# Kernel optimization log

Measured on AMD Instinct MI355X. Metric: run time of the kernel, lower is better.

The kernel has to match this reference:

```python
import jax, jax.numpy as jnp
import numpy as np


def _to_complex(x):
    # trailing axis holds (real, imag)
    return x[..., 0] + 1j * x[..., 1]


def _nufft2c(img, omega, csm):
    """Exact type-2 non-uniform DFT with coil sensitivities (reference for nufft2c_torch).

    img:   (H, W) real or complex image
    omega: (2, M) k-space coords in cycles/pixel, in [-0.5, 0.5]
    csm:   (C, H, W) complex coil sensitivity maps
    returns (C, M) complex k-space, centered & orthonormal-style 1/sqrt(HW) scaling.
    """
    H, W = img.shape
    y = jnp.arange(H, dtype=jnp.float32) - H / 2.0  # centered pixel coords
    z = jnp.arange(W, dtype=jnp.float32) - W / 2.0
    ey = jnp.exp(-2j * jnp.pi * omega[0][:, None] * y[None, :])  # (M, H)
    ez = jnp.exp(-2j * jnp.pi * omega[1][:, None] * z[None, :])  # (M, W)
    sim = csm * img[None, :, :].astype(csm.dtype)                # (C, H, W)
    tmp = jnp.einsum('chw,mw->cmh', sim, ez)                     # (C, M, H)
    k = jnp.einsum('cmh,mh->cm', tmp, ey) / np.float32(np.sqrt(H * W))
    return k


def setup_inputs() -> dict:
    key = jax.random.key(0)
    k0, k1, k2, k3, k4 = jax.random.split(key, 5)
    H = W = 300
    C = 4       # coils
    M = 4096    # non-Cartesian k-space samples
    img_pred = jax.random.normal(k0, (H, W, 1), jnp.float32)
    kdata = jax.random.normal(k1, (1, C, M, 2), jnp.float32)
    all_omega = jax.random.uniform(k2, (1, 2, M), jnp.float32) - 0.5  # cycles/pixel
    all_dcomp = jax.random.uniform(k3, (1, M), jnp.float32)
    all_csm = jax.random.normal(k4, (C, H, W, 2), jnp.float32)
    return {
        'img_pred': img_pred,
        'kdata': kdata,
        'all_omega': all_omega,
        'all_dcomp': all_dcomp,
        'all_csm': all_csm,
    }


def reference(img_pred, kdata, all_omega, all_dcomp, all_csm):
    Ncontrast = 1
    csm = _to_complex(all_csm)   # (C, H, W)
    kd = _to_complex(kdata)      # (Ncontrast, C, M)
    two_pi = jnp.float32(2.0 * np.pi)
    # radial k-space weighting, (Ncontrast, M)
    weight = jnp.sqrt((all_omega[:, 0, :] * two_pi) ** 2 +
                      (all_omega[:, 1, :] * two_pi) ** 2) + 1.0
    loss = jnp.float32(0.0)
    for ii in range(Ncontrast):
        img = img_pred[:, :, ii]                       # (H, W)
        ksp = _nufft2c(img, all_omega[ii], csm)        # (C, M)
        d = weight[ii][None, :] * (ksp - kd[ii])       # weighted complex residual
        # MSELoss over view_as_real == mean over all real & imag components
        loss = loss + jnp.mean(jnp.stack([d.real, d.imag]) ** 2)
    return loss
```

## Files before the change

kernel.cpp:

```cpp
#include <hip/hip_runtime.h>
#include <math.h>

#define HH 300
#define WW 300
#define CC 4
#define MM 4096
#define KP 640
#define NKC (KP/32)
#define CSTRIDE 384
#define MP (CC*CSTRIDE)
#define NP 8192
#define NRB (MP/128)

typedef __attribute__((ext_vector_type(4))) float f32x4;
typedef __attribute__((ext_vector_type(4))) int int4v;
typedef __attribute__((ext_vector_type(8))) int int8v;

#define TWO_PI 6.283185307179586f


__global__ __launch_bounds__(256) void prep_kernel(
    const float* __restrict__ img, const float* __restrict__ csm,
    const float* __restrict__ omega, unsigned char* __restrict__ A,
    unsigned char* __restrict__ B, float* __restrict__ out)
{
    const int bid = blockIdx.x;
    const int t   = threadIdx.x;
    if (bid == 0 && t == 0) out[0] = 0.0f;
    const int lane = t & 63;
    const int jj   = lane & 7;
    const int rl   = lane >> 3;

    if (bid < 960) {
        int gw = (bid * 256 + t) >> 6;
        int kc = gw / 192;
        int row = (gw - kc * 192) * 8 + rl;
        int k0 = kc * 32 + jj * 4;
        unsigned int word = 0;
        int c = row / CSTRIDE;
        int h = row - c * CSTRIDE;
        if (h < HH) {
            float v[4];
            #pragma unroll
            for (int q = 0; q < 4; ++q) {
                int k = k0 + q;
                float vv = 0.0f;
                if (k < 2 * WW) {
                    int w = (k < WW) ? k : k - WW;
                    float im = img[h * WW + w];
                    const float* cs = csm + (((size_t)c * HH + h) * WW + w) * 2;
                    vv = ((k < WW) ? cs[0] : cs[1]) * im;
                }
                v[q] = vv;
            }
            unsigned int lo = (unsigned int)(ushort)__builtin_amdgcn_cvt_pk_fp8_f32(v[0], v[1], 0, false);
            unsigned int hi = (unsigned int)(ushort)__builtin_amdgcn_cvt_pk_fp8_f32(v[2], v[3], 0, false);
            word = lo | (hi << 16);
        }
        *(unsigned int*)(A + ((size_t)kc * MP + row) * 32 + jj * 4) = word;
    } else {
        int gw = ((bid - 960) * 256 + t) >> 6;
        int kc = gw / 512;
        int m  = (gw - kc * 512) * 8 + rl;
        int k0 = kc * 32 + jj * 4;
        float om1 = omega[MM + m];
        float p0[4], p1[4];
        #pragma unroll
        for (int q = 0; q < 4; ++q) {
            int k = k0 + q;
            float a0 = 0.0f, a1 = 0.0f;
            if (k < 2 * WW) {
                int w = (k < WW) ? k : k - WW;
                float s, c;
                __sincosf(TWO_PI * om1 * (float)(w - 150), &s, &c);
                a0 = (k < WW) ? c : s;
                a1 = (k < WW) ? -s : c;
            }
            p0[q] = a0; p1[q] = a1;
        }
        unsigned int lo0 = (unsigned int)(ushort)__builtin_amdgcn_cvt_pk_fp8_f32(p0[0], p0[1], 0, false);
        unsigned int hi0 = (unsigned int)(ushort)__builtin_amdgcn_cvt_pk_fp8_f32(p0[2], p0[3], 0, false);
        unsigned int lo1 = (unsigned int)(ushort)__builtin_amdgcn_cvt_pk_fp8_f32(p1[0], p1[1], 0, false);
        unsigned int hi1 = (unsigned int)(ushort)__builtin_amdgcn_cvt_pk_fp8_f32(p1[2], p1[3], 0, false);
        *(unsigned int*)(B + ((size_t)kc * NP + m) * 32 + jj * 4)      = lo0 | (hi0 << 16);
        *(unsigned int*)(B + ((size_t)kc * NP + m + MM) * 32 + jj * 4) = lo1 | (hi1 << 16);
    }
}

__global__ __launch_bounds__(256, 3) void gemm_kernel(
    const unsigned char* __restrict__ A, const unsigned char* __restrict__ B,
    const float* __restrict__ omega, float2* __restrict__ P)
{
    __shared__ float2 red[128];

    const int t    = threadIdx.x;
    const int wave = t >> 6;
    const int ln   = t & 63;
    const int row0 = blockIdx.y * 128;
    const int col0 = blockIdx.x * 128;
    const int wr = wave >> 1, wc = wave & 1;
    const int lr = ln & 15;
    const int lq = ln >> 4;

    if (t < 128) red[t] = make_float2(0.0f, 0.0f);

    const int arow = row0 + wr * 64 + lr;
    const int bcol = col0 + wc * 64 + lr;

    f32x4 acc[4][4] = {};

    #pragma unroll
    for (int kc = 0; kc < NKC; kc += 4) {
        int8v a[4], b[4];
        #pragma unroll
        for (int i = 0; i < 4; ++i) {
            const unsigned char* pA = A + ((size_t)(kc + lq) * MP + arow + i * 16) * 32;
            int4v lo = *(const int4v*)pA;
            int4v hi = *(const int4v*)(pA + 16);
            a[i] = __builtin_shufflevector(lo, hi, 0, 1, 2, 3, 4, 5, 6, 7);
        }
        #pragma unroll
        for (int j = 0; j < 4; ++j) {
            const unsigned char* pB = B + ((size_t)(kc + lq) * NP + bcol + j * 16) * 32;
            int4v lo = *(const int4v*)pB;
            int4v hi = *(const int4v*)(pB + 16);
            b[j] = __builtin_shufflevector(lo, hi, 0, 1, 2, 3, 4, 5, 6, 7);
        }
        #pragma unroll
        for (int i = 0; i < 4; ++i)
            #pragma unroll
            for (int j = 0; j < 4; ++j)
                acc[i][j] = __builtin_amdgcn_mfma_scale_f32_16x16x128_f8f6f4(
                    a[i], b[j], acc[i][j], 0, 0,
                    0, 0x7f7f7f7f, 0, 0x7f7f7f7f);
    }

    __syncthreads();

    const int c  = row0 / CSTRIDE;
    const int h0 = row0 - c * CSTRIDE;

    #pragma unroll
    for (int j = 0; j < 4; ++j) {
        const int jcol = wc * 64 + j * 16 + lr;
        const int m = (col0 + jcol) & (MM - 1);
        const float om0 = omega[m];
        float ss, sc;
        __sincosf(TWO_PI * om0, &ss, &sc);
        const float str = sc, sti = -ss;
        float s2r = str * str - sti * sti, s2i = 2.0f * str * sti;
        float s4r = s2r * s2r - s2i * s2i, s4i = 2.0f * s2r * s2i;
        float s8r = s4r * s4r - s4i * s4i, s8i = 2.0f * s4r * s4i;
        float s16r = s8r * s8r - s8i * s8i, s16i = 2.0f * s8r * s8i;

        const int hb0 = h0 + wr * 64 + lq * 4;
        float sn, cs;
        __sincosf(TWO_PI * om0 * (float)(hb0 - 150), &sn, &cs);
        float byr = cs, byi = -sn;

        float pr = 0.0f, pi = 0.0f;
        #pragma unroll
        for (int i = 0; i < 4; ++i) {
            float er = byr, ei = byi;
            #pragma unroll
            for (int r = 0; r < 4; ++r) {
                const float v = acc[i][j][r];
                pr = fmaf(v, er, pr);
                pi = fmaf(v, ei, pi);
                float nr = er * str - ei * sti;
                ei = er * sti + ei * str;
                er = nr;
            }
            float nbr = byr * s16r - byi * s16i;
            byi = byr * s16i + byi * s16r;
            byr = nbr;
        }
        pr += __shfl_down(pr, 32); pi += __shfl_down(pi, 32);
        pr += __shfl_down(pr, 16); pi += __shfl_down(pi, 16);
        if (lq == 0) {
            atomicAdd(&red[jcol].x, pr);
            atomicAdd(&red[jcol].y, pi);
        }
    }
    __syncthreads();

    if (t < 128) {
        const int rb = row0 >> 7;
        P[(size_t)rb * NP + col0 + t] = red[t];
    }
}

__global__ __launch_bounds__(64) void loss_kernel(
    const float2* __restrict__ P, const float* __restrict__ kdata,
    const float* __restrict__ omega, float* __restrict__ out)
{
    const int t = blockIdx.x * 64 + threadIdx.x;
    const int c = t >> 12;
    const int m = t & (MM - 1);

    float kr = 0.0f, ki = 0.0f;
    #pragma unroll
    for (int q = 0; q < 3; ++q) {
        const int rb = 3 * c + q;
        float2 p0 = P[(size_t)rb * NP + m];
        float2 p1 = P[(size_t)rb * NP + m + MM];
        kr += p0.x - p1.y;
        ki += p0.y + p1.x;
    }
    kr *= (1.0f / 300.0f);
    ki *= (1.0f / 300.0f);

    const float om0 = omega[m];
    const float om1 = omega[MM + m];
    const size_t kidx = ((size_t)c * MM + m) * 2;
    const float kdr = kdata[kidx];
    const float kdi = kdata[kidx + 1];
    const float w0 = om0 * TWO_PI, w1 = om1 * TWO_PI;
    const float wg = sqrtf(w0 * w0 + w1 * w1) + 1.0f;
    const float dr = wg * (kr - kdr);
    const float di = wg * (ki - kdi);
    float val = (dr * dr + di * di) * (1.0f / (2.0f * CC * MM));

    #pragma unroll
    for (int off = 32; off > 0; off >>= 1) val += __shfl_down(val, off);
    if (threadIdx.x == 0) atomicAdd(out, val);
}

extern "C" void kernel_launch(void* const* d_in, const int* in_sizes, int n_in,
                              void* d_out, int out_size, void* d_ws, size_t ws_size,
                              hipStream_t stream) {
    const float* img   = (const float*)d_in[0];
    const float* kdata = (const float*)d_in[1];
    const float* omega = (const float*)d_in[2];
    const float* csm   = (const float*)d_in[4];
    float* out = (float*)d_out;

    unsigned char* Aws = (unsigned char*)d_ws;
    unsigned char* Bws = (unsigned char*)d_ws + (1u << 20);
    float2*        Pws = (float2*)((char*)d_ws + (8u << 20));

    prep_kernel<<<960 + 2560, 256, 0, stream>>>(img, csm, omega, Aws, Bws, out);
    gemm_kernel<<<dim3(NP / 128, MP / 128), 256, 0, stream>>>(Aws, Bws, omega, Pws);
    loss_kernel<<<CC * MM / 64, 64, 0, stream>>>(Pws, kdata, omega, out);
}
```

Before: 86.30 us.

## Use single-wave 64x64 GEMM blocks and skip padded row blocks

The GEMM now runs one wave per block on 64x64 tiles. It iterates over only 20 of the 24 row blocks, skipping the all-zero padding block (rows 320-383) of each coil. Each wave writes its partial sums directly to P, which removes the shared-memory atomics and both block barriers. The loss kernel now sums 5 partial blocks per coil instead of 3. The cost is less data reuse per block (A and B tiles are fetched by more blocks) in exchange for less padded work and more, smaller blocks.

```diff
diff --git a/kernel.cpp b/kernel.cpp
--- a/kernel.cpp
+++ b/kernel.cpp
@@ -10,7 +10,6 @@
 #define CSTRIDE 384
 #define MP (CC*CSTRIDE)
 #define NP 8192
-#define NRB (MP/128)
 
 typedef __attribute__((ext_vector_type(4))) float f32x4;
 typedef __attribute__((ext_vector_type(4))) int int4v;
@@ -87,25 +86,17 @@
     }
 }
 
-__global__ __launch_bounds__(256, 3) void gemm_kernel(
+__global__ __launch_bounds__(64, 4) void gemm_kernel(
     const unsigned char* __restrict__ A, const unsigned char* __restrict__ B,
     const float* __restrict__ omega, float2* __restrict__ P)
 {
-    __shared__ float2 red[128];
-
-    const int t    = threadIdx.x;
-    const int wave = t >> 6;
-    const int ln   = t & 63;
-    const int row0 = blockIdx.y * 128;
-    const int col0 = blockIdx.x * 128;
-    const int wr = wave >> 1, wc = wave & 1;
-    const int lr = ln & 15;
-    const int lq = ln >> 4;
-
-    if (t < 128) red[t] = make_float2(0.0f, 0.0f);
-
-    const int arow = row0 + wr * 64 + lr;
-    const int bcol = col0 + wc * 64 + lr;
+    const int ln   = threadIdx.x;
+    const int lr   = ln & 15;
+    const int lq   = ln >> 4;
+    const int y    = blockIdx.y;
+    const int rbp  = y + y / 5;
+    const int row0 = rbp * 64;
+    const int col0 = blockIdx.x * 64;
 
     f32x4 acc[4][4] = {};
 
@@ -114,14 +105,14 @@
         int8v a[4], b[4];
         #pragma unroll
         for (int i = 0; i < 4; ++i) {
-            const unsigned char* pA = A + ((size_t)(kc + lq) * MP + arow + i * 16) * 32;
+            const unsigned char* pA = A + ((size_t)(kc + lq) * MP + row0 + i * 16 + lr) * 32;
             int4v lo = *(const int4v*)pA;
             int4v hi = *(const int4v*)(pA + 16);
             a[i] = __builtin_shufflevector(lo, hi, 0, 1, 2, 3, 4, 5, 6, 7);
         }
         #pragma unroll
         for (int j = 0; j < 4; ++j) {
-            const unsigned char* pB = B + ((size_t)(kc + lq) * NP + bcol + j * 16) * 32;
+            const unsigned char* pB = B + ((size_t)(kc + lq) * NP + col0 + j * 16 + lr) * 32;
             int4v lo = *(const int4v*)pB;
             int4v hi = *(const int4v*)(pB + 16);
             b[j] = __builtin_shufflevector(lo, hi, 0, 1, 2, 3, 4, 5, 6, 7);
@@ -135,15 +126,12 @@
                     0, 0x7f7f7f7f, 0, 0x7f7f7f7f);
     }
 
-    __syncthreads();
-
-    const int c  = row0 / CSTRIDE;
-    const int h0 = row0 - c * CSTRIDE;
+    const int h0 = (rbp % 6) * 64;
 
     #pragma unroll
     for (int j = 0; j < 4; ++j) {
-        const int jcol = wc * 64 + j * 16 + lr;
-        const int m = (col0 + jcol) & (MM - 1);
+        const int col = col0 + j * 16 + lr;
+        const int m = col & (MM - 1);
         const float om0 = omega[m];
         float ss, sc;
         __sincosf(TWO_PI * om0, &ss, &sc);
@@ -153,7 +141,7 @@
         float s8r = s4r * s4r - s4i * s4i, s8i = 2.0f * s4r * s4i;
         float s16r = s8r * s8r - s8i * s8i, s16i = 2.0f * s8r * s8i;
 
-        const int hb0 = h0 + wr * 64 + lq * 4;
+        const int hb0 = h0 + lq * 4;
         float sn, cs;
         __sincosf(TWO_PI * om0 * (float)(hb0 - 150), &sn, &cs);
         float byr = cs, byi = -sn;
@@ -177,16 +165,8 @@
         }
         pr += __shfl_down(pr, 32); pi += __shfl_down(pi, 32);
         pr += __shfl_down(pr, 16); pi += __shfl_down(pi, 16);
-        if (lq == 0) {
-            atomicAdd(&red[jcol].x, pr);
-            atomicAdd(&red[jcol].y, pi);
-        }
-    }
-    __syncthreads();
-
-    if (t < 128) {
-        const int rb = row0 >> 7;
-        P[(size_t)rb * NP + col0 + t] = red[t];
+        if (lq == 0)
+            P[(size_t)y * NP + col] = make_float2(pr, pi);
     }
 }
 
@@ -200,10 +180,10 @@
 
     float kr = 0.0f, ki = 0.0f;
     #pragma unroll
-    for (int q = 0; q < 3; ++q) {
-        const int rb = 3 * c + q;
-        float2 p0 = P[(size_t)rb * NP + m];
-        float2 p1 = P[(size_t)rb * NP + m + MM];
+    for (int q = 0; q < 5; ++q) {
+        const int y = 5 * c + q;
+        float2 p0 = P[(size_t)y * NP + m];
+        float2 p1 = P[(size_t)y * NP + m + MM];
         kr += p0.x - p1.y;
         ki += p0.y + p1.x;
     }
@@ -240,6 +220,6 @@
     float2*        Pws = (float2*)((char*)d_ws + (8u << 20));
 
     prep_kernel<<<960 + 2560, 256, 0, stream>>>(img, csm, omega, Aws, Bws, out);
-    gemm_kernel<<<dim3(NP / 128, MP / 128), 256, 0, stream>>>(Aws, Bws, omega, Pws);
+    gemm_kernel<<<dim3(NP / 64, 20), 64, 0, stream>>>(Aws, Bws, omega, Pws);
     loss_kernel<<<CC * MM / 64, 64, 0, stream>>>(Pws, kdata, omega, out);
 }
```

New measurement: 97.76 us. +13.3%, slower.

## Store FP8 operands in MFMA fragment order for coalesced 16-byte loads

Applied to the files above, without the earlier changes.

The prep kernel now writes A and B in a per-fragment layout: each 16-row by 128-k block occupies 2048 contiguous bytes arranged so each lane's two 16-byte halves sit at ln*16 and ln*16+1024. The GEMM loads each operand fragment as two fully contiguous wave-wide 1KB reads instead of strided 32-byte rows per k-chunk, which is meant to improve global/L2 access efficiency. The GEMM launch bound also drops the min-3-blocks occupancy hint, giving the compiler more register freedom at the risk of lower occupancy.

```diff
diff --git a/kernel.cpp b/kernel.cpp
--- a/kernel.cpp
+++ b/kernel.cpp
@@ -6,11 +6,12 @@
 #define CC 4
 #define MM 4096
 #define KP 640
-#define NKC (KP/32)
+#define NKG (KP/128)
 #define CSTRIDE 384
 #define MP (CC*CSTRIDE)
 #define NP 8192
 #define NRB (MP/128)
+#define BHALF (2621440)
 
 typedef __attribute__((ext_vector_type(4))) float f32x4;
 typedef __attribute__((ext_vector_type(4))) int int4v;
@@ -27,18 +28,23 @@
     const int bid = blockIdx.x;
     const int t   = threadIdx.x;
     if (bid == 0 && t == 0) out[0] = 0.0f;
-    const int lane = t & 63;
-    const int jj   = lane & 7;
-    const int rl   = lane >> 3;
 
     if (bid < 960) {
-        int gw = (bid * 256 + t) >> 6;
-        int kc = gw / 192;
-        int row = (gw - kc * 192) * 8 + rl;
-        int k0 = kc * 32 + jj * 4;
+        const int gid = bid * 256 + t;
+        const int L   = gid * 4;
+        const int fragidx = L >> 11;
+        const int o  = L & 2047;
+        const int hf = (o >> 10) & 1;
+        const int ch = (o >> 8) & 3;
+        const int lr = (o >> 4) & 15;
+        const int b0 = o & 15;
+        const int row16 = fragidx / NKG;
+        const int g     = fragidx - row16 * NKG;
+        const int row = row16 * 16 + lr;
+        const int k0  = g * 128 + ch * 32 + hf * 16 + b0;
+        const int c = row / CSTRIDE;
+        const int h = row - c * CSTRIDE;
         unsigned int word = 0;
-        int c = row / CSTRIDE;
-        int h = row - c * CSTRIDE;
         if (h < HH) {
             float v[4];
             #pragma unroll
@@ -57,13 +63,21 @@
             unsigned int hi = (unsigned int)(ushort)__builtin_amdgcn_cvt_pk_fp8_f32(v[2], v[3], 0, false);
             word = lo | (hi << 16);
         }
-        *(unsigned int*)(A + ((size_t)kc * MP + row) * 32 + jj * 4) = word;
+        *(unsigned int*)(A + L) = word;
     } else {
-        int gw = ((bid - 960) * 256 + t) >> 6;
-        int kc = gw / 512;
-        int m  = (gw - kc * 512) * 8 + rl;
-        int k0 = kc * 32 + jj * 4;
-        float om1 = omega[MM + m];
+        const int gid = (bid - 960) * 256 + t;
+        const int L   = gid * 4;
+        const int fragidx = L >> 11;
+        const int o  = L & 2047;
+        const int hf = (o >> 10) & 1;
+        const int ch = (o >> 8) & 3;
+        const int lr = (o >> 4) & 15;
+        const int b0 = o & 15;
+        const int m16 = fragidx / NKG;
+        const int g   = fragidx - m16 * NKG;
+        const int m  = m16 * 16 + lr;
+        const int k0 = g * 128 + ch * 32 + hf * 16 + b0;
+        const float om1 = omega[MM + m];
         float p0[4], p1[4];
         #pragma unroll
         for (int q = 0; q < 4; ++q) {
@@ -82,12 +96,12 @@
         unsigned int hi0 = (unsigned int)(ushort)__builtin_amdgcn_cvt_pk_fp8_f32(p0[2], p0[3], 0, false);
         unsigned int lo1 = (unsigned int)(ushort)__builtin_amdgcn_cvt_pk_fp8_f32(p1[0], p1[1], 0, false);
         unsigned int hi1 = (unsigned int)(ushort)__builtin_amdgcn_cvt_pk_fp8_f32(p1[2], p1[3], 0, false);
-        *(unsigned int*)(B + ((size_t)kc * NP + m) * 32 + jj * 4)      = lo0 | (hi0 << 16);
-        *(unsigned int*)(B + ((size_t)kc * NP + m + MM) * 32 + jj * 4) = lo1 | (hi1 << 16);
-    }
-}
-
-__global__ __launch_bounds__(256, 3) void gemm_kernel(
+        *(unsigned int*)(B + L)          = lo0 | (hi0 << 16);
+        *(unsigned int*)(B + BHALF + L)  = lo1 | (hi1 << 16);
+    }
+}
+
+__global__ __launch_bounds__(256) void gemm_kernel(
     const unsigned char* __restrict__ A, const unsigned char* __restrict__ B,
     const float* __restrict__ omega, float2* __restrict__ P)
 {
@@ -104,26 +118,26 @@
 
     if (t < 128) red[t] = make_float2(0.0f, 0.0f);
 
-    const int arow = row0 + wr * 64 + lr;
-    const int bcol = col0 + wc * 64 + lr;
+    const int fA0 = (row0 >> 4) + wr * 4;
+    const int fB0 = (col0 >> 4) + wc * 4;
 
     f32x4 acc[4][4] = {};
 
     #pragma unroll
-    for (int kc = 0; kc < NKC; kc += 4) {
+    for (int g = 0; g < NKG; ++g) {
         int8v a[4], b[4];
         #pragma unroll
         for (int i = 0; i < 4; ++i) {
-            const unsigned char* pA = A + ((size_t)(kc + lq) * MP + arow + i * 16) * 32;
+            const unsigned char* pA = A + (((size_t)(fA0 + i) * NKG + g) << 11) + ln * 16;
             int4v lo = *(const int4v*)pA;
-            int4v hi = *(const int4v*)(pA + 16);
+            int4v hi = *(const int4v*)(pA + 1024);
             a[i] = __builtin_shufflevector(lo, hi, 0, 1, 2, 3, 4, 5, 6, 7);
         }
         #pragma unroll
         for (int j = 0; j < 4; ++j) {
-            const unsigned char* pB = B + ((size_t)(kc + lq) * NP + bcol + j * 16) * 32;
+            const unsigned char* pB = B + (((size_t)(fB0 + j) * NKG + g) << 11) + ln * 16;
             int4v lo = *(const int4v*)pB;
-            int4v hi = *(const int4v*)(pB + 16);
+            int4v hi = *(const int4v*)(pB + 1024);
             b[j] = __builtin_shufflevector(lo, hi, 0, 1, 2, 3, 4, 5, 6, 7);
         }
         #pragma unroll
```

Result: slower. 88.81 us (+2.9%).
